# Kernel optimization log

Hardware: AMD Instinct MI355X
Metric: run time of the kernel (lower is better)

## Reference

```python
import jax, jax.numpy as jnp
import numpy as np

BS = 2
EMBED = 256
NH = 8
NL = 4
NP = 4
HD = EMBED // NH
SHAPES = [(128, 128), (64, 64), (32, 32), (16, 16)]
NQ = sum(h * w for h, w in SHAPES)  # 21760


def setup_inputs() -> dict:
    key = jax.random.key(0)
    ks = jax.random.split(key, 12)
    s = 1.0 / np.sqrt(EMBED)
    return {
        "query": jax.random.normal(ks[0], (BS, NQ, EMBED), jnp.float32),
        "reference_points": jax.random.uniform(ks[1], (BS, NQ, NL, 2), jnp.float32),
        "value": jax.random.normal(ks[2], (BS, NQ, EMBED), jnp.float32),
        "W_off": jax.random.normal(ks[3], (EMBED, NH * NL * NP * 2), jnp.float32) * 0.01,
        "b_off": jax.random.normal(ks[4], (NH * NL * NP * 2,), jnp.float32) * 0.5,
        "W_attn": jax.random.normal(ks[5], (EMBED, NH * NL * NP), jnp.float32) * 0.02,
        "b_attn": jnp.zeros((NH * NL * NP,), jnp.float32),
        "W_v": jax.random.normal(ks[6], (EMBED, EMBED), jnp.float32) * s,
        "b_v": jnp.zeros((EMBED,), jnp.float32),
        "W_out": jax.random.normal(ks[7], (EMBED, EMBED), jnp.float32) * s,
        "b_out": jnp.zeros((EMBED,), jnp.float32),
        "value_spatial_shapes": np.asarray(SHAPES, dtype=np.int64),
    }


def _ms_deform_attn(value, shapes, loc, aw):
    # value: [bs,V,nh,d]; loc: [bs,nq,nh,L,P,2] in [0,1]; aw: [bs,nq,nh,L,P]
    bs, V, nh, d = value.shape
    nq = loc.shape[1]
    out = jnp.zeros((bs, nq, nh, d), value.dtype)
    start = 0
    b_idx = jnp.arange(bs)[:, None, None, None]
    h_idx = jnp.arange(nh)[None, None, :, None]
    for l, (H, W) in enumerate(shapes):
        H, W = int(H), int(W)
        v = value[:, start:start + H * W].reshape(bs, H, W, nh, d)
        start += H * W
        g = 2.0 * loc[:, :, :, l] - 1.0  # [bs,nq,nh,P,2], grid_sample convention
        # align_corners=False pixel coordinates
        x = ((g[..., 0] + 1.0) * W - 1.0) * 0.5
        y = ((g[..., 1] + 1.0) * H - 1.0) * 0.5
        x0 = jnp.floor(x); y0 = jnp.floor(y)
        wx1 = x - x0; wx0 = 1.0 - wx1
        wy1 = y - y0; wy0 = 1.0 - wy1

        def gather(yi, xi):
            inb = (yi >= 0) & (yi < H) & (xi >= 0) & (xi < W)
            yc = jnp.clip(yi, 0, H - 1).astype(jnp.int32)
            xc = jnp.clip(xi, 0, W - 1).astype(jnp.int32)
            vals = v[b_idx, yc, xc, h_idx]  # [bs,nq,nh,P,d]
            return vals * inb[..., None].astype(v.dtype)

        samp = (gather(y0, x0) * (wy0 * wx0)[..., None]
                + gather(y0, x0 + 1) * (wy0 * wx1)[..., None]
                + gather(y0 + 1, x0) * (wy1 * wx0)[..., None]
                + gather(y0 + 1, x0 + 1) * (wy1 * wx1)[..., None])
        out = out + jnp.einsum('bqhpd,bqhp->bqhd', samp, aw[:, :, :, l])
    return out.reshape(bs, nq, nh * d)


def reference(query, reference_points, value, W_off, b_off, W_attn, b_attn,
              W_v, b_v, W_out, b_out, value_spatial_shapes):
    shapes = np.asarray(value_spatial_shapes)  # static [L,2]
    bs, nq, _ = query.shape
    v = (value @ W_v + b_v).reshape(bs, -1, NH, HD)
    off = (query @ W_off + b_off).reshape(bs, nq, NH, NL, NP, 2)
    aw = (query @ W_attn + b_attn).reshape(bs, nq, NH, NL * NP)
    aw = jax.nn.softmax(aw, axis=-1).reshape(bs, nq, NH, NL, NP)
    # offset normalizer: (W,H) per level
    norm = jnp.asarray(shapes[:, ::-1].astype(np.float32))  # [L,2]
    loc = reference_points[:, :, None, :, None, :] + off / norm[None, None, None, :, None, :]
    out = _ms_deform_attn(v, shapes, loc, aw)
    return out @ W_out + b_out
```

## Files before the change

### kernel.cpp

```cpp
#include <hip/hip_runtime.h>
#include <math.h>

#define BS 2
#define NQ 21760
#define V_LEN 21760
#define EMBED 256
#define NH 8
#define NL 4
#define NP 4
#define HD 32

typedef _Float16 f16;
typedef _Float16 half8 __attribute__((ext_vector_type(8)));
typedef _Float16 half4v __attribute__((ext_vector_type(4)));
typedef float f32x4 __attribute__((ext_vector_type(4)));

__device__ __forceinline__ void load_lds16(const void* g, void* l) {
    __builtin_amdgcn_global_load_lds(
        (const __attribute__((address_space(1))) void*)g,
        (__attribute__((address_space(3))) void*)l, 16, 0, 0);
}

__global__ __launch_bounds__(256) void prep(
    const float* __restrict__ W_v, const float* __restrict__ W_off,
    const float* __restrict__ W_attn, const float* __restrict__ W_out,
    const float* __restrict__ b_off, const float* __restrict__ b_attn,
    f16* __restrict__ WTv, f16* __restrict__ WToa, f16* __restrict__ WTu,
    float* __restrict__ bcat)
{
    const int nb = blockIdx.x;
    const int k = threadIdx.x;
    if (nb < 256) {
        WTv[nb * 256 + k] = (f16)W_v[k * 256 + nb];
    } else if (nb < 640) {
        int j = nb - 256;
        float w = (j < 256) ? W_off[k * 256 + j] : W_attn[k * 128 + (j - 256)];
        WToa[j * 256 + k] = (f16)w;
    } else if (nb < 896) {
        int j = nb - 640;
        WTu[j * 256 + k] = (f16)W_out[k * 256 + j];
    } else if (nb == 896) {
        bcat[k] = b_off[k];
        if (k < 128) bcat[256 + k] = b_attn[k];
    }
}

template<bool AF16>
__device__ __forceinline__ void gemm128_core(
    const void* __restrict__ Av, const f16* __restrict__ WT,
    const float* __restrict__ bias, void* __restrict__ Cv,
    int N, int bm, int bn, bool outF16)
{
    const int K = 256;
    __shared__ __align__(16) f16 As[4 * 128 * 8];
    __shared__ __align__(16) f16 Bs[4 * 128 * 8];

    const int tid = threadIdx.x;
    const int lane = tid & 63, wv = tid >> 6;
    const int wr = wv >> 1, wc = wv & 1;
    const int quad = lane >> 4, l16 = lane & 15;

    f32x4 acc[4][4];
    #pragma unroll
    for (int i = 0; i < 4; i++)
        #pragma unroll
        for (int j = 0; j < 4; j++)
            acc[i][j] = (f32x4){0.f, 0.f, 0.f, 0.f};

    for (int k0 = 0; k0 < K; k0 += 32) {
        #pragma unroll
        for (int i = 0; i < 2; i++) {
            int S0 = (i * 4 + wv) * 64;
            int S = S0 + lane;
            int col = S & 127, kcg = S >> 7;
            load_lds16(&WT[(size_t)(bn + col) * K + k0 + kcg * 8], &Bs[S0 * 8]);
        }
        if constexpr (AF16) {
            const f16* A = (const f16*)Av;
            #pragma unroll
            for (int i = 0; i < 2; i++) {
                int S0 = (i * 4 + wv) * 64;
                int S = S0 + lane;
                int row = S & 127, kcg = S >> 7;
                load_lds16(&A[(size_t)(bm + row) * K + k0 + kcg * 8], &As[S0 * 8]);
            }
        } else {
            const float* A = (const float*)Av;
            #pragma unroll
            for (int i = 0; i < 4; i++) {
                int F = i * 256 + tid;
                int row = F >> 3, kq = F & 7;
                float4 f = *(const float4*)&A[(size_t)(bm + row) * K + k0 + kq * 4];
                half4v h;
                h[0] = (f16)f.x; h[1] = (f16)f.y; h[2] = (f16)f.z; h[3] = (f16)f.w;
                *(half4v*)&As[((kq >> 1) * 128 + row) * 8 + (kq & 1) * 4] = h;
            }
        }
        __syncthreads();

        half8 af[4], bf[4];
        #pragma unroll
        for (int mi = 0; mi < 4; mi++)
            af[mi] = *(const half8*)&As[(quad * 128 + wr * 64 + mi * 16 + l16) * 8];
        #pragma unroll
        for (int ni = 0; ni < 4; ni++)
            bf[ni] = *(const half8*)&Bs[(quad * 128 + wc * 64 + ni * 16 + l16) * 8];
        #pragma unroll
        for (int mi = 0; mi < 4; mi++)
            #pragma unroll
            for (int ni = 0; ni < 4; ni++)
                acc[mi][ni] = __builtin_amdgcn_mfma_f32_16x16x32_f16(
                    af[mi], bf[ni], acc[mi][ni], 0, 0, 0);
        __syncthreads();
    }

    #pragma unroll
    for (int mi = 0; mi < 4; mi++) {
        #pragma unroll
        for (int ni = 0; ni < 4; ni++) {
            const int col = bn + wc * 64 + ni * 16 + l16;
            const int row0 = bm + wr * 64 + mi * 16 + quad * 4;
            const float bc = bias[col];
            if (outF16) {
                #pragma unroll
                for (int r = 0; r < 4; r++)
                    ((f16*)Cv)[(size_t)(row0 + r) * N + col] = (f16)(acc[mi][ni][r] + bc);
            } else {
                #pragma unroll
                for (int r = 0; r < 4; r++)
                    ((float*)Cv)[(size_t)(row0 + r) * N + col] = acc[mi][ni][r] + bc;
            }
        }
    }
}

__global__ __launch_bounds__(256) void front_gemm(
    const float* __restrict__ value, const float* __restrict__ query,
    const f16* __restrict__ WTv, const f16* __restrict__ WToa,
    const float* __restrict__ b_v, const float* __restrict__ bcat,
    f16* __restrict__ vproj, float* __restrict__ offaw)
{
    int bid = blockIdx.x;
    if (bid < 680) {
        int bnt = bid & 1, bmt = bid >> 1;
        gemm128_core<false>(value, WTv, b_v, vproj, 256, bmt * 128, bnt * 128, true);
    } else {
        int b2 = bid - 680;
        int bnt = b2 % 3, bmt = b2 / 3;
        gemm128_core<false>(query, WToa, bcat, offaw, 384, bmt * 128, bnt * 128, false);
    }
}

__global__ __launch_bounds__(256) void out_gemm(
    const f16* __restrict__ samp, const f16* __restrict__ WTu,
    const float* __restrict__ b_out, float* __restrict__ out)
{
    int bnt = blockIdx.x & 1, bmt = blockIdx.x >> 1;
    gemm128_core<true>(samp, WTu, b_out, out, 256, bmt * 128, bnt * 128, false);
}

__global__ __launch_bounds__(256) void deform_sample(
    const f16* __restrict__ vproj, const float* __restrict__ offaw,
    const float* __restrict__ refp, f16* __restrict__ sampled)
{
    const int wv = threadIdx.x >> 6;
    const int lane = threadIdx.x & 63;
    const int q = blockIdx.x * 4 + wv;
    const int b = blockIdx.y;
    const int bq = b * NQ + q;

    __shared__ float s_off[4][256];
    __shared__ float s_aw[4][128];
    __shared__ __align__(16) f16  s_w[4][128][4];
    __shared__ __align__(16) int  s_idx[4][128][4];

    const float* row = offaw + (size_t)bq * 384;
    #pragma unroll
    for (int i = 0; i < 4; i++) s_off[wv][lane + i * 64] = row[lane + i * 64];
    #pragma unroll
    for (int i = 0; i < 2; i++) s_aw[wv][lane + i * 64] = row[256 + lane + i * 64];
    __syncthreads();

    if (lane < 8) {
        float m = -1e30f;
        #pragma unroll
        for (int i = 0; i < 16; i++) m = fmaxf(m, s_aw[wv][lane * 16 + i]);
        float ssum = 0.f;
        #pragma unroll
        for (int i = 0; i < 16; i++) {
            float e = __expf(s_aw[wv][lane * 16 + i] - m);
            s_aw[wv][lane * 16 + i] = e;
            ssum += e;
        }
        float r = 1.0f / ssum;
        #pragma unroll
        for (int i = 0; i < 16; i++) s_aw[wv][lane * 16 + i] *= r;
    }
    __syncthreads();

    #pragma unroll
    for (int sI = 0; sI < 2; sI++) {
        int d = lane + sI * 64;
        int h = d & 7, lp = d >> 3, l = lp >> 2, p = lp & 3;
        int Wl = 128 >> l;
        int st = (l == 0) ? 0 : (l == 1) ? 16384 : (l == 2) ? 20480 : 21504;
        float rx = refp[(size_t)bq * 8 + l * 2 + 0];
        float ry = refp[(size_t)bq * 8 + l * 2 + 1];
        float ox = s_off[wv][((h * NL + l) * NP + p) * 2 + 0];
        float oy = s_off[wv][((h * NL + l) * NP + p) * 2 + 1];
        float fW = (float)Wl;
        float x = (rx + ox / fW) * fW - 0.5f;
        float y = (ry + oy / fW) * fW - 0.5f;
        float xf = floorf(x), yf = floorf(y);
        int x0 = (int)xf, y0 = (int)yf;
        float wx1 = x - xf, wx0 = 1.f - wx1;
        float wy1 = y - yf, wy0 = 1.f - wy1;
        float aw = s_aw[wv][h * 16 + lp];
        bool vx0 = (x0 >= 0) && (x0 < Wl);
        bool vx1 = (x0 + 1 >= 0) && (x0 + 1 < Wl);
        bool vy0 = (y0 >= 0) && (y0 < Wl);
        bool vy1 = (y0 + 1 >= 0) && (y0 + 1 < Wl);
        int cx0 = min(max(x0, 0), Wl - 1), cx1 = min(max(x0 + 1, 0), Wl - 1);
        int cy0 = min(max(y0, 0), Wl - 1), cy1 = min(max(y0 + 1, 0), Wl - 1);
        half4v w4;
        w4[0] = (f16)((vy0 && vx0) ? wy0 * wx0 * aw : 0.f);
        w4[1] = (f16)((vy0 && vx1) ? wy0 * wx1 * aw : 0.f);
        w4[2] = (f16)((vy1 && vx0) ? wy1 * wx0 * aw : 0.f);
        w4[3] = (f16)((vy1 && vx1) ? wy1 * wx1 * aw : 0.f);
        *(half4v*)&s_w[wv][d][0] = w4;
        int4 i4;
        i4.x = (st + cy0 * Wl + cx0) << 9;
        i4.y = (st + cy0 * Wl + cx1) << 9;
        i4.z = (st + cy1 * Wl + cx0) << 9;
        i4.w = (st + cy1 * Wl + cx1) << 9;
        *(int4*)&s_idx[wv][d][0] = i4;
    }
    __syncthreads();

    const int h = lane >> 3;
    const unsigned int cb = (unsigned int)lane * 8u;
    const char* vb = (const char*)(vproj + (size_t)b * V_LEN * EMBED);
    float a0 = 0.f, a1 = 0.f, a2 = 0.f, a3 = 0.f;
    #pragma unroll 8
    for (int lp = 0; lp < 16; lp++) {
        const int d = lp * 8 + h;
        const half4v w4 = *(const half4v*)&s_w[wv][d][0];
        const int4  i4 = *(const int4*)&s_idx[wv][d][0];
        half4v v0 = *(const half4v*)(vb + ((unsigned int)i4.x + cb));
        half4v v1 = *(const half4v*)(vb + ((unsigned int)i4.y + cb));
        half4v v2 = *(const half4v*)(vb + ((unsigned int)i4.z + cb));
        half4v v3 = *(const half4v*)(vb + ((unsigned int)i4.w + cb));
        a0 += (float)w4[0] * (float)v0[0] + (float)w4[1] * (float)v1[0] + (float)w4[2] * (float)v2[0] + (float)w4[3] * (float)v3[0];
        a1 += (float)w4[0] * (float)v0[1] + (float)w4[1] * (float)v1[1] + (float)w4[2] * (float)v2[1] + (float)w4[3] * (float)v3[1];
        a2 += (float)w4[0] * (float)v0[2] + (float)w4[1] * (float)v1[2] + (float)w4[2] * (float)v2[2] + (float)w4[3] * (float)v3[2];
        a3 += (float)w4[0] * (float)v0[3] + (float)w4[1] * (float)v1[3] + (float)w4[2] * (float)v2[3] + (float)w4[3] * (float)v3[3];
    }

    half4v o;
    o[0] = (f16)a0; o[1] = (f16)a1; o[2] = (f16)a2; o[3] = (f16)a3;
    *(half4v*)&sampled[(size_t)bq * 256 + lane * 4] = o;
}

extern "C" void kernel_launch(void* const* d_in, const int* in_sizes, int n_in,
                              void* d_out, int out_size, void* d_ws, size_t ws_size,
                              hipStream_t stream)
{
    const float* query  = (const float*)d_in[0];
    const float* refp   = (const float*)d_in[1];
    const float* value  = (const float*)d_in[2];
    const float* W_off  = (const float*)d_in[3];
    const float* b_off  = (const float*)d_in[4];
    const float* W_attn = (const float*)d_in[5];
    const float* b_attn = (const float*)d_in[6];
    const float* W_v    = (const float*)d_in[7];
    const float* b_v    = (const float*)d_in[8];
    const float* W_out  = (const float*)d_in[9];
    const float* b_out  = (const float*)d_in[10];
    float* out = (float*)d_out;

    const int M = BS * NQ;

    char* ws = (char*)d_ws;
    f16*   WTv   = (f16*)ws;    ws += 256 * 256 * 2;
    f16*   WToa  = (f16*)ws;    ws += 384 * 256 * 2;
    f16*   WTu   = (f16*)ws;    ws += 256 * 256 * 2;
    float* bcat  = (float*)ws;  ws += 384 * 4 + 128;
    f16*   vproj = (f16*)ws;    ws += (size_t)M * 256 * 2;
    float* offaw = (float*)ws;  ws += (size_t)M * 384 * 4;
    f16*   samp  = (f16*)ws;    ws += (size_t)M * 256 * 2;

    prep<<<897, 256, 0, stream>>>(W_v, W_off, W_attn, W_out, b_off, b_attn,
                                  WTv, WToa, WTu, bcat);
    front_gemm<<<1700, 256, 0, stream>>>(value, query, WTv, WToa, b_v, bcat,
                                         vproj, offaw);
    deform_sample<<<dim3(NQ / 4, BS), 256, 0, stream>>>(vproj, offaw, refp, samp);
    out_gemm<<<680, 256, 0, stream>>>(samp, WTu, b_out, out);
}
```

Before: 311.6 us.

## Use head-major value layout with paired-corner loads, direct-from-global MFMA GEMMs

Adds a separate cast kernel that converts value and query to fp16 up front. The GEMMs now feed MFMA fragments straight from global memory instead of staging through LDS with barriers. The value projection is written head-major ([b,h,V,32]), so the deform sampler can fetch both x-neighbour corners with one 16-byte load per row, using two indices instead of four plus a shuffle reduction. This cuts gather instructions and LDS sync, at the cost of an extra cast pass, uncoalesced direct loads in the GEMMs, and reliance on padding for x=-1 and x=W reads.

```diff
diff --git a/kernel.cpp b/kernel.cpp
--- a/kernel.cpp
+++ b/kernel.cpp
@@ -9,16 +9,29 @@
 #define NL 4
 #define NP 4
 #define HD 32
+#define M_TOT (BS * NQ)
+#define MN (M_TOT * EMBED)
+#define VPAD 256
 
 typedef _Float16 f16;
 typedef _Float16 half8 __attribute__((ext_vector_type(8)));
 typedef _Float16 half4v __attribute__((ext_vector_type(4)));
 typedef float f32x4 __attribute__((ext_vector_type(4)));
 
-__device__ __forceinline__ void load_lds16(const void* g, void* l) {
-    __builtin_amdgcn_global_load_lds(
-        (const __attribute__((address_space(1))) void*)g,
-        (__attribute__((address_space(3))) void*)l, 16, 0, 0);
+__global__ __launch_bounds__(256) void cast2(
+    const float* __restrict__ value, const float* __restrict__ query,
+    f16* __restrict__ vq16)
+{
+    const int n4 = MN / 4;
+    int i = blockIdx.x * 256 + threadIdx.x;
+    const float4* s;
+    int j;
+    if (i < n4) { s = (const float4*)value; j = i; }
+    else        { s = (const float4*)query; j = i - n4; }
+    float4 f = s[j];
+    half4v h;
+    h[0] = (f16)f.x; h[1] = (f16)f.y; h[2] = (f16)f.z; h[3] = (f16)f.w;
+    ((half4v*)vq16)[i] = h;
 }
 
 __global__ __launch_bounds__(256) void prep(
@@ -45,21 +58,20 @@
     }
 }
 
-template<bool AF16>
-__device__ __forceinline__ void gemm128_core(
-    const void* __restrict__ Av, const f16* __restrict__ WT,
-    const float* __restrict__ bias, void* __restrict__ Cv,
-    int N, int bm, int bn, bool outF16)
-{
-    const int K = 256;
-    __shared__ __align__(16) f16 As[4 * 128 * 8];
-    __shared__ __align__(16) f16 Bs[4 * 128 * 8];
-
+template<int OUTMODE>
+__device__ __forceinline__ void gemm_direct(
+    const f16* __restrict__ A, const f16* __restrict__ WT,
+    const float* __restrict__ bias, float* __restrict__ Cf,
+    f16* __restrict__ Ch, int N, int bm, int bn)
+{
     const int tid = threadIdx.x;
     const int lane = tid & 63, wv = tid >> 6;
     const int wr = wv >> 1, wc = wv & 1;
     const int quad = lane >> 4, l16 = lane & 15;
 
+    const f16* Ap = A  + (size_t)(bm + wr * 64 + l16) * 256 + quad * 8;
+    const f16* Bp = WT + (size_t)(bn + wc * 64 + l16) * 256 + quad * 8;
+
     f32x4 acc[4][4];
     #pragma unroll
     for (int i = 0; i < 4; i++)
@@ -67,53 +79,24 @@
         for (int j = 0; j < 4; j++)
             acc[i][j] = (f32x4){0.f, 0.f, 0.f, 0.f};
 
-    for (int k0 = 0; k0 < K; k0 += 32) {
-        #pragma unroll
-        for (int i = 0; i < 2; i++) {
-            int S0 = (i * 4 + wv) * 64;
-            int S = S0 + lane;
-            int col = S & 127, kcg = S >> 7;
-            load_lds16(&WT[(size_t)(bn + col) * K + k0 + kcg * 8], &Bs[S0 * 8]);
-        }
-        if constexpr (AF16) {
-            const f16* A = (const f16*)Av;
-            #pragma unroll
-            for (int i = 0; i < 2; i++) {
-                int S0 = (i * 4 + wv) * 64;
-                int S = S0 + lane;
-                int row = S & 127, kcg = S >> 7;
-                load_lds16(&A[(size_t)(bm + row) * K + k0 + kcg * 8], &As[S0 * 8]);
-            }
-        } else {
-            const float* A = (const float*)Av;
-            #pragma unroll
-            for (int i = 0; i < 4; i++) {
-                int F = i * 256 + tid;
-                int row = F >> 3, kq = F & 7;
-                float4 f = *(const float4*)&A[(size_t)(bm + row) * K + k0 + kq * 4];
-                half4v h;
-                h[0] = (f16)f.x; h[1] = (f16)f.y; h[2] = (f16)f.z; h[3] = (f16)f.w;
-                *(half4v*)&As[((kq >> 1) * 128 + row) * 8 + (kq & 1) * 4] = h;
-            }
-        }
-        __syncthreads();
-
+    #pragma unroll
+    for (int ks = 0; ks < 8; ks++) {
         half8 af[4], bf[4];
         #pragma unroll
         for (int mi = 0; mi < 4; mi++)
-            af[mi] = *(const half8*)&As[(quad * 128 + wr * 64 + mi * 16 + l16) * 8];
+            af[mi] = *(const half8*)(Ap + mi * 16 * 256 + ks * 32);
         #pragma unroll
         for (int ni = 0; ni < 4; ni++)
-            bf[ni] = *(const half8*)&Bs[(quad * 128 + wc * 64 + ni * 16 + l16) * 8];
+            bf[ni] = *(const half8*)(Bp + ni * 16 * 256 + ks * 32);
         #pragma unroll
         for (int mi = 0; mi < 4; mi++)
             #pragma unroll
             for (int ni = 0; ni < 4; ni++)
                 acc[mi][ni] = __builtin_amdgcn_mfma_f32_16x16x32_f16(
                     af[mi], bf[ni], acc[mi][ni], 0, 0, 0);
-        __syncthreads();
-    }
-
+    }
+
+    const int bb = (bm >= NQ) ? 1 : 0;
     #pragma unroll
     for (int mi = 0; mi < 4; mi++) {
         #pragma unroll
@@ -121,33 +104,36 @@
             const int col = bn + wc * 64 + ni * 16 + l16;
             const int row0 = bm + wr * 64 + mi * 16 + quad * 4;
             const float bc = bias[col];
-            if (outF16) {
+            if constexpr (OUTMODE == 0) {
                 #pragma unroll
                 for (int r = 0; r < 4; r++)
-                    ((f16*)Cv)[(size_t)(row0 + r) * N + col] = (f16)(acc[mi][ni][r] + bc);
+                    Cf[(size_t)(row0 + r) * N + col] = acc[mi][ni][r] + bc;
             } else {
+                const int v0 = row0 - bb * NQ;
+                const size_t hb = (size_t)(bb * 8 + (col >> 5)) * V_LEN;
+                const int c = col & 31;
                 #pragma unroll
                 for (int r = 0; r < 4; r++)
-                    ((float*)Cv)[(size_t)(row0 + r) * N + col] = acc[mi][ni][r] + bc;
+                    Ch[(hb + v0 + r) * 32 + c] = (f16)(acc[mi][ni][r] + bc);
             }
         }
     }
 }
 
 __global__ __launch_bounds__(256) void front_gemm(
-    const float* __restrict__ value, const float* __restrict__ query,
-    const f16* __restrict__ WTv, const f16* __restrict__ WToa,
-    const float* __restrict__ b_v, const float* __restrict__ bcat,
-    f16* __restrict__ vproj, float* __restrict__ offaw)
+    const f16* __restrict__ vq16, const f16* __restrict__ WTv,
+    const f16* __restrict__ WToa, const float* __restrict__ b_v,
+    const float* __restrict__ bcat, f16* __restrict__ vp,
+    float* __restrict__ offaw)
 {
     int bid = blockIdx.x;
     if (bid < 680) {
         int bnt = bid & 1, bmt = bid >> 1;
-        gemm128_core<false>(value, WTv, b_v, vproj, 256, bmt * 128, bnt * 128, true);
+        gemm_direct<2>(vq16, WTv, b_v, nullptr, vp, 256, bmt * 128, bnt * 128);
     } else {
         int b2 = bid - 680;
         int bnt = b2 % 3, bmt = b2 / 3;
-        gemm128_core<false>(query, WToa, bcat, offaw, 384, bmt * 128, bnt * 128, false);
+        gemm_direct<0>(vq16 + MN, WToa, bcat, offaw, nullptr, 384, bmt * 128, bnt * 128);
     }
 }
 
@@ -156,11 +142,11 @@
     const float* __restrict__ b_out, float* __restrict__ out)
 {
     int bnt = blockIdx.x & 1, bmt = blockIdx.x >> 1;
-    gemm128_core<true>(samp, WTu, b_out, out, 256, bmt * 128, bnt * 128, false);
+    gemm_direct<0>(samp, WTu, b_out, out, nullptr, 256, bmt * 128, bnt * 128);
 }
 
 __global__ __launch_bounds__(256) void deform_sample(
-    const f16* __restrict__ vproj, const float* __restrict__ offaw,
+    const f16* __restrict__ vp, const float* __restrict__ offaw,
     const float* __restrict__ refp, f16* __restrict__ sampled)
 {
     const int wv = threadIdx.x >> 6;
@@ -171,8 +157,8 @@
 
     __shared__ float s_off[4][256];
     __shared__ float s_aw[4][128];
-    __shared__ __align__(16) f16  s_w[4][128][4];
-    __shared__ __align__(16) int  s_idx[4][128][4];
+    __shared__ __align__(8)  f16 s_w[4][128][4];
+    __shared__ __align__(8)  int s_idx[4][128][2];
 
     const float* row = offaw + (size_t)bq * 384;
     #pragma unroll
@@ -220,45 +206,47 @@
         bool vx1 = (x0 + 1 >= 0) && (x0 + 1 < Wl);
         bool vy0 = (y0 >= 0) && (y0 < Wl);
         bool vy1 = (y0 + 1 >= 0) && (y0 + 1 < Wl);
-        int cx0 = min(max(x0, 0), Wl - 1), cx1 = min(max(x0 + 1, 0), Wl - 1);
         int cy0 = min(max(y0, 0), Wl - 1), cy1 = min(max(y0 + 1, 0), Wl - 1);
+        int xc  = min(max(x0, -1), Wl - 1);
         half4v w4;
         w4[0] = (f16)((vy0 && vx0) ? wy0 * wx0 * aw : 0.f);
         w4[1] = (f16)((vy0 && vx1) ? wy0 * wx1 * aw : 0.f);
         w4[2] = (f16)((vy1 && vx0) ? wy1 * wx0 * aw : 0.f);
         w4[3] = (f16)((vy1 && vx1) ? wy1 * wx1 * aw : 0.f);
         *(half4v*)&s_w[wv][d][0] = w4;
-        int4 i4;
-        i4.x = (st + cy0 * Wl + cx0) << 9;
-        i4.y = (st + cy0 * Wl + cx1) << 9;
-        i4.z = (st + cy1 * Wl + cx0) << 9;
-        i4.w = (st + cy1 * Wl + cx1) << 9;
-        *(int4*)&s_idx[wv][d][0] = i4;
+        int2 i2;
+        i2.x = (st + cy0 * Wl + xc) << 6;
+        i2.y = (st + cy1 * Wl + xc) << 6;
+        *(int2*)&s_idx[wv][d][0] = i2;
     }
     __syncthreads();
 
-    const int h = lane >> 3;
-    const unsigned int cb = (unsigned int)lane * 8u;
-    const char* vb = (const char*)(vproj + (size_t)b * V_LEN * EMBED);
-    float a0 = 0.f, a1 = 0.f, a2 = 0.f, a3 = 0.f;
-    #pragma unroll 8
+    const int h = lane >> 3, j = lane & 7;
+    const int jo = j * 16;
+    const char* vb = (const char*)vp + (size_t)(b * 8 + h) * (V_LEN * 64);
+    float a[8] = {0.f, 0.f, 0.f, 0.f, 0.f, 0.f, 0.f, 0.f};
+    #pragma unroll 4
     for (int lp = 0; lp < 16; lp++) {
         const int d = lp * 8 + h;
+        const int2 i2 = *(const int2*)&s_idx[wv][d][0];
         const half4v w4 = *(const half4v*)&s_w[wv][d][0];
-        const int4  i4 = *(const int4*)&s_idx[wv][d][0];
-        half4v v0 = *(const half4v*)(vb + ((unsigned int)i4.x + cb));
-        half4v v1 = *(const half4v*)(vb + ((unsigned int)i4.y + cb));
-        half4v v2 = *(const half4v*)(vb + ((unsigned int)i4.z + cb));
-        half4v v3 = *(const half4v*)(vb + ((unsigned int)i4.w + cb));
-        a0 += (float)w4[0] * (float)v0[0] + (float)w4[1] * (float)v1[0] + (float)w4[2] * (float)v2[0] + (float)w4[3] * (float)v3[0];
-        a1 += (float)w4[0] * (float)v0[1] + (float)w4[1] * (float)v1[1] + (float)w4[2] * (float)v2[1] + (float)w4[3] * (float)v3[1];
-        a2 += (float)w4[0] * (float)v0[2] + (float)w4[1] * (float)v1[2] + (float)w4[2] * (float)v2[2] + (float)w4[3] * (float)v3[2];
-        a3 += (float)w4[0] * (float)v0[3] + (float)w4[1] * (float)v1[3] + (float)w4[2] * (float)v2[3] + (float)w4[3] * (float)v3[3];
-    }
-
-    half4v o;
-    o[0] = (f16)a0; o[1] = (f16)a1; o[2] = (f16)a2; o[3] = (f16)a3;
-    *(half4v*)&sampled[(size_t)bq * 256 + lane * 4] = o;
+        half8 v0 = *(const half8*)(vb + (i2.x + jo));
+        half8 v1 = *(const half8*)(vb + (i2.y + jo));
+        float w0 = (float)(j < 4 ? w4[0] : w4[1]);
+        float w1 = (float)(j < 4 ? w4[2] : w4[3]);
+        #pragma unroll
+        for (int c = 0; c < 8; c++)
+            a[c] += w0 * (float)v0[c] + w1 * (float)v1[c];
+    }
+    #pragma unroll
+    for (int c = 0; c < 8; c++) a[c] += __shfl_xor(a[c], 4, 64);
+
+    if (j < 4) {
+        half8 o;
+        #pragma unroll
+        for (int c = 0; c < 8; c++) o[c] = (f16)a[c];
+        *(half8*)&sampled[(size_t)bq * 256 + h * 32 + j * 8] = o;
+    }
 }
 
 extern "C" void kernel_launch(void* const* d_in, const int* in_sizes, int n_in,
@@ -278,21 +266,21 @@
     const float* b_out  = (const float*)d_in[10];
     float* out = (float*)d_out;
 
-    const int M = BS * NQ;
-
     char* ws = (char*)d_ws;
     f16*   WTv   = (f16*)ws;    ws += 256 * 256 * 2;
     f16*   WToa  = (f16*)ws;    ws += 384 * 256 * 2;
     f16*   WTu   = (f16*)ws;    ws += 256 * 256 * 2;
-    float* bcat  = (float*)ws;  ws += 384 * 4 + 128;
-    f16*   vproj = (f16*)ws;    ws += (size_t)M * 256 * 2;
-    float* offaw = (float*)ws;  ws += (size_t)M * 384 * 4;
-    f16*   samp  = (f16*)ws;    ws += (size_t)M * 256 * 2;
-
+    float* bcat  = (float*)ws;  ws += 384 * 4 + 512;
+    f16*   vq16  = (f16*)ws;    ws += (size_t)2 * MN * 2;
+    ws += VPAD;
+    f16*   vp    = (f16*)ws;    ws += (size_t)MN * 2 + VPAD;
+    float* offaw = (float*)ws;  ws += (size_t)M_TOT * 384 * 4;
+    f16*   samp  = (f16*)ws;    ws += (size_t)MN * 2;
+
+    cast2<<<2 * MN / 4 / 256, 256, 0, stream>>>(value, query, vq16);
     prep<<<897, 256, 0, stream>>>(W_v, W_off, W_attn, W_out, b_off, b_attn,
                                   WTv, WToa, WTu, bcat);
-    front_gemm<<<1700, 256, 0, stream>>>(value, query, WTv, WToa, b_v, bcat,
-                                         vproj, offaw);
-    deform_sample<<<dim3(NQ / 4, BS), 256, 0, stream>>>(vproj, offaw, refp, samp);
+    front_gemm<<<1700, 256, 0, stream>>>(vq16, WTv, WToa, b_v, bcat, vp, offaw);
+    deform_sample<<<dim3(NQ / 4, BS), 256, 0, stream>>>(vp, offaw, refp, samp);
     out_gemm<<<680, 256, 0, stream>>>(samp, WTu, b_out, out);
 }
```

Measured after the change: 315.4 us. About the same (+1.2%).
